# Performance work log

Hardware: AMD Instinct MI355X
Metric: run time of the kernel (lower is better)

## Reference

```python
import jax, jax.numpy as jnp
import numpy as np

NEG = 1e12  # matches the torch '-inf' surrogate value


def _sinusoidal_pos(seq_len, dim):
    # bert4keras-style: pe[..., 0::2] = sin, pe[..., 1::2] = cos
    pos = jnp.arange(seq_len, dtype=jnp.float32)
    i = jnp.arange(dim // 2, dtype=jnp.float32)
    freq = jnp.power(10000.0, -2.0 * i / dim)
    ang = pos[:, None] * freq[None, :]                      # [S, dim/2]
    pe = jnp.stack([jnp.sin(ang), jnp.cos(ang)], axis=-1)   # [S, dim/2, 2]
    return pe.reshape(seq_len, dim)                          # [S, dim]


def _rope(e, cos_pos, sin_pos):
    # additional_part = stack([-e[...,1::2], e[...,::2]], -1).reshape(e.shape)
    rot = jnp.stack([-e[..., 1::2], e[..., 0::2]], axis=-1).reshape(e.shape)
    return e * cos_pos + rot * sin_pos


def setup_inputs() -> dict:
    key = jax.random.key(0)
    k = jax.random.split(key, 5)
    B, S, H, inner, L = 8, 512, 768, 64, 16
    x = jax.random.normal(k[0], (B, S, H), dtype=jnp.float32)
    W1 = jax.random.normal(k[1], (H, 2 * inner), dtype=jnp.float32) * 0.02
    b1 = jnp.zeros((2 * inner,), dtype=jnp.float32)
    W2 = jax.random.normal(k[2], (H, 2 * L), dtype=jnp.float32) * 0.02
    b2 = jnp.zeros((2 * L,), dtype=jnp.float32)
    attention_mask = jnp.ones((B, S), dtype=jnp.int32)
    return {"x": x, "W1": W1, "b1": b1, "W2": W2, "b2": b2,
            "attention_mask": attention_mask}


def reference(x, W1, b1, W2, b2, attention_mask):
    B, S, H = x.shape
    inner = W1.shape[1] // 2

    t = x @ W1 + b1                                 # [B,S,2*inner]
    start_token = t[..., 0::2]                      # [B,S,inner]
    end_token = t[..., 1::2]                        # [B,S,inner]

    pe = _sinusoidal_pos(S, inner)[None]            # [1,S,inner]
    cos_pos = jnp.repeat(pe[..., 1::2], 2, axis=-1)
    sin_pos = jnp.repeat(pe[..., 0::2], 2, axis=-1)
    start_token = _rope(start_token, cos_pos, sin_pos)
    end_token = _rope(end_token, cos_pos, sin_pos)

    span_score = jnp.einsum('bmd,bnd->bmn', start_token, end_token) / (inner ** 0.5)

    typing = jnp.swapaxes(x @ W2 + b2, 1, 2) / 2.0  # [B,2L,S]

    # entity_score: [B, L, S(start), S(end)]
    entity_score = (span_score[:, None]
                    + typing[:, 0::2, None, :]
                    + typing[:, 1::2, :, None])

    m = attention_mask.astype(entity_score.dtype)
    m_row = m[:, None, :, None]                     # mask over start axis
    m_col = m[:, None, None, :]                     # mask over end axis
    entity_score = entity_score * m_row + (-NEG) * (1.0 - m_row)
    entity_score = entity_score * m_col + (-NEG) * (1.0 - m_col)

    tril = jnp.tril(jnp.ones((S, S), entity_score.dtype), k=-1)
    entity_score = entity_score - tril * NEG
    return entity_score
```

## Files before the change

kernel.cpp:

```cpp
#include <hip/hip_runtime.h>

#define NEGF 1.0e12f

constexpr int Hdim = 768;
constexpr int NC   = 160;
constexpr int ROWS = 4096;
constexpr int SEQ  = 512;
constexpr int KSPLIT = 4;

typedef __attribute__((ext_vector_type(8))) short  short8;
typedef __attribute__((ext_vector_type(4))) float  floatx4;

__device__ inline unsigned short f2bf(float f) {
    union { float f; unsigned u; } v; v.f = f;
    return (unsigned short)((v.u + 0x8000u) >> 16);
}

__global__ __launch_bounds__(256) void gemm_mfma_k(
    const float* __restrict__ x, const float* __restrict__ W1,
    const float* __restrict__ W2, float* __restrict__ partial)
{
    __shared__ __align__(16) unsigned short xs[64 * 40];
    __shared__ __align__(16) unsigned short ws[NC * 40];

    const int tid  = threadIdx.x;
    const int wave = tid >> 6;
    const int lane = tid & 63;
    const int quad = lane >> 4;
    const int nl   = lane & 15;
    const int r0   = blockIdx.x * 64;
    const int k0   = blockIdx.y * 192;

    floatx4 acc[10];
#pragma unroll
    for (int t = 0; t < 10; t++) acc[t] = (floatx4)(0.0f);

    for (int kt = 0; kt < 192; kt += 32) {
        const int kb = k0 + kt;
        {
            const int row = tid >> 2;
            const int kq  = (tid & 3) * 8;
            const float* xp = x + (size_t)(r0 + row) * Hdim + kb + kq;
            float4 v0 = *(const float4*)xp;
            float4 v1 = *(const float4*)(xp + 4);
            short8 sv;
            sv[0] = (short)f2bf(v0.x); sv[1] = (short)f2bf(v0.y);
            sv[2] = (short)f2bf(v0.z); sv[3] = (short)f2bf(v0.w);
            sv[4] = (short)f2bf(v1.x); sv[5] = (short)f2bf(v1.y);
            sv[6] = (short)f2bf(v1.z); sv[7] = (short)f2bf(v1.w);
            *(short8*)(xs + row * 40 + kq) = sv;
        }
#pragma unroll
        for (int g = 0; g < 3; g++) {
            const int c   = g * 64 + (tid & 63);
            const int kq2 = (tid >> 6) * 8;
            if (c < NC) {
                float f[8];
                if (c < 128) {
                    const float* wp = W1 + (size_t)(kb + kq2) * 128 + c;
#pragma unroll
                    for (int j = 0; j < 8; j++) f[j] = wp[j * 128];
                } else {
                    const float* wp = W2 + (size_t)(kb + kq2) * 32 + (c - 128);
#pragma unroll
                    for (int j = 0; j < 8; j++) f[j] = wp[j * 32];
                }
                short8 sv;
#pragma unroll
                for (int j = 0; j < 8; j++) sv[j] = (short)f2bf(f[j]);
                *(short8*)(ws + c * 40 + kq2) = sv;
            }
        }
        __syncthreads();

        short8 af = *(const short8*)(xs + (wave * 16 + nl) * 40 + quad * 8);
#pragma unroll
        for (int t = 0; t < 10; t++) {
            short8 bf = *(const short8*)(ws + (t * 16 + nl) * 40 + quad * 8);
            acc[t] = __builtin_amdgcn_mfma_f32_16x16x32_bf16(af, bf, acc[t], 0, 0, 0);
        }
        __syncthreads();
    }

    float* pout = partial + (size_t)blockIdx.y * ROWS * NC;
#pragma unroll
    for (int t = 0; t < 10; t++) {
#pragma unroll
        for (int r = 0; r < 4; r++) {
            pout[(size_t)(r0 + wave * 16 + quad * 4 + r) * NC + t * 16 + nl] = acc[t][r];
        }
    }
}

__global__ __launch_bounds__(256) void combine_rope_k(
    const float* __restrict__ partial, const float* __restrict__ b1,
    const float* __restrict__ b2, unsigned short* __restrict__ startbf,
    unsigned short* __restrict__ endbf, float* __restrict__ tyn,
    float* __restrict__ tym)
{
    const int tid = threadIdx.x;
    const int row = blockIdx.x * 4 + (tid >> 6);
    const int u   = tid & 63;
    const int b   = row >> 9;
    const int s   = row & 511;
    const float* p0 = partial + (size_t)row * NC;
    const size_t cstride = (size_t)ROWS * NC;

    if (u < 32) {
        const int i = u;
        float4 a0 = *(const float4*)(p0 + 4 * i);
        float4 a1 = *(const float4*)(p0 + cstride + 4 * i);
        float4 a2 = *(const float4*)(p0 + 2 * cstride + 4 * i);
        float4 a3 = *(const float4*)(p0 + 3 * cstride + 4 * i);
        float t0 = a0.x + a1.x + a2.x + a3.x + b1[4 * i + 0];
        float t1 = a0.y + a1.y + a2.y + a3.y + b1[4 * i + 1];
        float t2 = a0.z + a1.z + a2.z + a3.z + b1[4 * i + 2];
        float t3 = a0.w + a1.w + a2.w + a3.w + b1[4 * i + 3];
        float freq = __powf(10000.0f, -(float)i * (1.0f / 32.0f));
        float ang  = (float)s * freq;
        float sn, cs;
        __sincosf(ang, &sn, &cs);
        float so0 = (t0 * cs - t2 * sn) * 0.125f;
        float so1 = (t2 * cs + t0 * sn) * 0.125f;
        float eo0 = t1 * cs - t3 * sn;
        float eo1 = t3 * cs + t1 * sn;
        ushort2 sp; sp.x = f2bf(so0); sp.y = f2bf(so1);
        ushort2 ep; ep.x = f2bf(eo0); ep.y = f2bf(eo1);
        *(ushort2*)(startbf + (size_t)row * 64 + 2 * i) = sp;
        *(ushort2*)(endbf   + (size_t)row * 64 + 2 * i) = ep;
    } else {
        const int j = u - 32;
        float t = p0[128 + j] + p0[cstride + 128 + j] + p0[2 * cstride + 128 + j]
                + p0[3 * cstride + 128 + j] + b2[j];
        float v = t * 0.5f;
        const int l = j >> 1;
        if ((j & 1) == 0) tyn[((size_t)b * 16 + l) * SEQ + s] = v;
        else              tym[((size_t)b * 16 + l) * SEQ + s] = v;
    }
}

__global__ __launch_bounds__(256) void entity_k(
    const unsigned short* __restrict__ startbf, const unsigned short* __restrict__ endbf,
    const float* __restrict__ tyn, const float* __restrict__ tym,
    const int* __restrict__ amask, float* __restrict__ out)
{
    __shared__ __align__(16) unsigned short sA[64 * 72];
    __shared__ __align__(16) unsigned short sB[64 * 72];
    __shared__ float tyn_s[16 * 64];
    __shared__ float tym_s[16 * 64];
    __shared__ float mrow_s[64];
    __shared__ float mcol_s[64];

    const int tid = threadIdx.x;
    const int b   = blockIdx.z;
    const int m0  = blockIdx.y * 64;
    const int n0  = blockIdx.x * 64;

    for (int t = tid; t < 512; t += 256) {
        int row = t >> 3;
        int kq  = (t & 7) * 8;
        *(short8*)(sA + row * 72 + kq) =
            *(const short8*)(startbf + (size_t)(b * SEQ + m0 + row) * 64 + kq);
        *(short8*)(sB + row * 72 + kq) =
            *(const short8*)(endbf + (size_t)(b * SEQ + n0 + row) * 64 + kq);
    }
    for (int t = tid; t < 16 * 64; t += 256) {
        int l = t >> 6, i = t & 63;
        tym_s[t] = tym[((size_t)b * 16 + l) * SEQ + m0 + i];
        tyn_s[t] = tyn[((size_t)b * 16 + l) * SEQ + n0 + i];
    }
    if (tid < 64)       mrow_s[tid] = (float)amask[b * SEQ + m0 + tid];
    else if (tid < 128) mcol_s[tid - 64] = (float)amask[b * SEQ + n0 + (tid - 64)];
    __syncthreads();

    const int wave = tid >> 6;
    const int lane = tid & 63;
    const int quad = lane >> 4;
    const int nl   = lane & 15;

    short8 a0 = *(const short8*)(sA + (wave * 16 + nl) * 72 + quad * 8);
    short8 a1 = *(const short8*)(sA + (wave * 16 + nl) * 72 + 32 + quad * 8);

    floatx4 acc[4];
#pragma unroll
    for (int t = 0; t < 4; t++) acc[t] = (floatx4)(0.0f);
#pragma unroll
    for (int t = 0; t < 4; t++) {
        short8 bf0 = *(const short8*)(sB + (t * 16 + nl) * 72 + quad * 8);
        short8 bf1 = *(const short8*)(sB + (t * 16 + nl) * 72 + 32 + quad * 8);
        acc[t] = __builtin_amdgcn_mfma_f32_16x16x32_bf16(a0, bf0, acc[t], 0, 0, 0);
        acc[t] = __builtin_amdgcn_mfma_f32_16x16x32_bf16(a1, bf1, acc[t], 0, 0, 0);
    }

    float mr[4], radd[4];
#pragma unroll
    for (int r = 0; r < 4; r++) {
        mr[r]   = mrow_s[wave * 16 + quad * 4 + r];
        radd[r] = -NEGF * (1.0f - mr[r]);
    }
    float mc[4], cadd[4];
#pragma unroll
    for (int t = 0; t < 4; t++) {
        mc[t]   = mcol_s[t * 16 + nl];
        cadd[t] = -NEGF * (1.0f - mc[t]);
    }
    const bool lower = (m0 > n0);
    const bool diag  = (m0 == n0);
    const int  lm    = wave * 16 + quad * 4;

    for (int l = 0; l < 16; l++) {
        float tmv[4];
#pragma unroll
        for (int r = 0; r < 4; r++) tmv[r] = tym_s[l * 64 + lm + r];
        float* ob = out + ((size_t)(b * 16 + l) * SEQ + m0 + lm) * SEQ + n0;
#pragma unroll
        for (int t = 0; t < 4; t++) {
            float tnv = tyn_s[l * 64 + t * 16 + nl];
#pragma unroll
            for (int r = 0; r < 4; r++) {
                float v = acc[t][r] + tnv + tmv[r];
                v = v * mr[r] + radd[r];
                v = v * mc[t] + cadd[t];
                if (lower) v -= NEGF;
                else if (diag && (lm + r > t * 16 + nl)) v -= NEGF;
                ob[(size_t)r * SEQ + t * 16 + nl] = v;
            }
        }
    }
}

extern "C" void kernel_launch(void* const* d_in, const int* in_sizes, int n_in,
                              void* d_out, int out_size, void* d_ws, size_t ws_size,
                              hipStream_t stream) {
    const float* x     = (const float*)d_in[0];
    const float* W1    = (const float*)d_in[1];
    const float* b1    = (const float*)d_in[2];
    const float* W2    = (const float*)d_in[3];
    const float* b2    = (const float*)d_in[4];
    const int*   amask = (const int*)d_in[5];
    float* out = (float*)d_out;

    char* base = (char*)d_ws;
    float*          partial = (float*)base;
    unsigned short* startbf = (unsigned short*)(base + 10485760);
    unsigned short* endbf   = (unsigned short*)(base + 10485760 + 524288);
    float*          tyn     = (float*)(base + 10485760 + 2 * 524288);
    float*          tym     = (float*)(base + 10485760 + 2 * 524288 + 262144);

    hipLaunchKernelGGL(gemm_mfma_k, dim3(64, KSPLIT), dim3(256), 0, stream,
                       x, W1, W2, partial);
    hipLaunchKernelGGL(combine_rope_k, dim3(ROWS / 4), dim3(256), 0, stream,
                       partial, b1, b2, startbf, endbf, tyn, tym);
    hipLaunchKernelGGL(entity_k, dim3(8, 8, 8), dim3(256), 0, stream,
                       startbf, endbf, tyn, tym, amask, out);
}
```

Baseline: 168.2 us.

## Fuse projection GEMM with RoPE epilogue, drop split-K, and prefetch operands

Replaces the split-K GEMM plus a separate combine/RoPE kernel with one kernel. Each block covers 32 rows over the full K dimension, register-prefetches the next K tile while doing MFMA on the current one, and applies bias, RoPE and typing in an LDS epilogue. This removes the 10MB partial-sum round trip and one launch, but leaves only 128 blocks, which may underfill the GPU. The entity output writes also become nontemporal stores.

```diff
diff --git a/kernel.cpp b/kernel.cpp
--- a/kernel.cpp
+++ b/kernel.cpp
@@ -6,7 +6,6 @@
 constexpr int NC   = 160;
 constexpr int ROWS = 4096;
 constexpr int SEQ  = 512;
-constexpr int KSPLIT = 4;
 
 typedef __attribute__((ext_vector_type(8))) short  short8;
 typedef __attribute__((ext_vector_type(4))) float  floatx4;
@@ -16,126 +15,133 @@
     return (unsigned short)((v.u + 0x8000u) >> 16);
 }
 
-__global__ __launch_bounds__(256) void gemm_mfma_k(
+__global__ __launch_bounds__(256) void gemm_rope_fused_k(
     const float* __restrict__ x, const float* __restrict__ W1,
-    const float* __restrict__ W2, float* __restrict__ partial)
+    const float* __restrict__ b1, const float* __restrict__ W2,
+    const float* __restrict__ b2, unsigned short* __restrict__ startbf,
+    unsigned short* __restrict__ endbf, float* __restrict__ tyn,
+    float* __restrict__ tym)
 {
-    __shared__ __align__(16) unsigned short xs[64 * 40];
+    __shared__ __align__(16) unsigned short xs[32 * 40];
     __shared__ __align__(16) unsigned short ws[NC * 40];
+    __shared__ __align__(16) float ts[32 * 160];
 
     const int tid  = threadIdx.x;
     const int wave = tid >> 6;
     const int lane = tid & 63;
     const int quad = lane >> 4;
     const int nl   = lane & 15;
-    const int r0   = blockIdx.x * 64;
-    const int k0   = blockIdx.y * 192;
-
-    floatx4 acc[10];
-#pragma unroll
-    for (int t = 0; t < 10; t++) acc[t] = (floatx4)(0.0f);
-
-    for (int kt = 0; kt < 192; kt += 32) {
-        const int kb = k0 + kt;
+    const int rg   = wave >> 1;
+    const int cgp  = wave & 1;
+    const int r0   = blockIdx.x * 32;
+
+    const int c0  = tid % 160,         kq0 = (tid / 160) * 8;
+    const int c1  = (tid + 256) % 160, kq1 = ((tid + 256) / 160) * 8;
+    const int c2  = (tid + 512) % 160, kq2 = ((tid + 512) / 160) * 8;
+    const int xrow = tid >> 3;
+    const int xk4  = (tid & 7) * 4;
+
+    floatx4 acc[5];
+#pragma unroll
+    for (int t = 0; t < 5; t++) acc[t] = (floatx4)(0.0f);
+
+    float4 xv;
+    float  wf0[8], wf1[8], wf2[8];
+
+    auto loadW8 = [&](int c, int kq, int kb, float* f) {
+        if (c < 128) {
+            const float* wp = W1 + (size_t)(kb + kq) * 128 + c;
+#pragma unroll
+            for (int j = 0; j < 8; j++) f[j] = wp[(size_t)j * 128];
+        } else {
+            const float* wp = W2 + (size_t)(kb + kq) * 32 + (c - 128);
+#pragma unroll
+            for (int j = 0; j < 8; j++) f[j] = wp[(size_t)j * 32];
+        }
+    };
+
+    xv = *(const float4*)(x + (size_t)(r0 + xrow) * Hdim + 0 + xk4);
+    loadW8(c0, kq0, 0, wf0);
+    loadW8(c1, kq1, 0, wf1);
+    if (tid < 128) loadW8(c2, kq2, 0, wf2);
+
+    for (int kt = 0; kt < 24; kt++) {
         {
-            const int row = tid >> 2;
-            const int kq  = (tid & 3) * 8;
-            const float* xp = x + (size_t)(r0 + row) * Hdim + kb + kq;
-            float4 v0 = *(const float4*)xp;
-            float4 v1 = *(const float4*)(xp + 4);
-            short8 sv;
-            sv[0] = (short)f2bf(v0.x); sv[1] = (short)f2bf(v0.y);
-            sv[2] = (short)f2bf(v0.z); sv[3] = (short)f2bf(v0.w);
-            sv[4] = (short)f2bf(v1.x); sv[5] = (short)f2bf(v1.y);
-            sv[6] = (short)f2bf(v1.z); sv[7] = (short)f2bf(v1.w);
-            *(short8*)(xs + row * 40 + kq) = sv;
-        }
-#pragma unroll
-        for (int g = 0; g < 3; g++) {
-            const int c   = g * 64 + (tid & 63);
-            const int kq2 = (tid >> 6) * 8;
-            if (c < NC) {
-                float f[8];
-                if (c < 128) {
-                    const float* wp = W1 + (size_t)(kb + kq2) * 128 + c;
-#pragma unroll
-                    for (int j = 0; j < 8; j++) f[j] = wp[j * 128];
-                } else {
-                    const float* wp = W2 + (size_t)(kb + kq2) * 32 + (c - 128);
-#pragma unroll
-                    for (int j = 0; j < 8; j++) f[j] = wp[j * 32];
-                }
-                short8 sv;
-#pragma unroll
-                for (int j = 0; j < 8; j++) sv[j] = (short)f2bf(f[j]);
-                *(short8*)(ws + c * 40 + kq2) = sv;
+            short4 sv;
+            sv.x = (short)f2bf(xv.x); sv.y = (short)f2bf(xv.y);
+            sv.z = (short)f2bf(xv.z); sv.w = (short)f2bf(xv.w);
+            *(short4*)(xs + xrow * 40 + xk4) = sv;
+            short8 s0, s1, s2;
+#pragma unroll
+            for (int j = 0; j < 8; j++) { s0[j] = (short)f2bf(wf0[j]); s1[j] = (short)f2bf(wf1[j]); }
+            *(short8*)(ws + c0 * 40 + kq0) = s0;
+            *(short8*)(ws + c1 * 40 + kq1) = s1;
+            if (tid < 128) {
+#pragma unroll
+                for (int j = 0; j < 8; j++) s2[j] = (short)f2bf(wf2[j]);
+                *(short8*)(ws + c2 * 40 + kq2) = s2;
             }
         }
         __syncthreads();
 
-        short8 af = *(const short8*)(xs + (wave * 16 + nl) * 40 + quad * 8);
-#pragma unroll
-        for (int t = 0; t < 10; t++) {
-            short8 bf = *(const short8*)(ws + (t * 16 + nl) * 40 + quad * 8);
+        if (kt < 23) {
+            const int kb = (kt + 1) * 32;
+            xv = *(const float4*)(x + (size_t)(r0 + xrow) * Hdim + kb + xk4);
+            loadW8(c0, kq0, kb, wf0);
+            loadW8(c1, kq1, kb, wf1);
+            if (tid < 128) loadW8(c2, kq2, kb, wf2);
+        }
+
+        short8 af = *(const short8*)(xs + (rg * 16 + nl) * 40 + quad * 8);
+#pragma unroll
+        for (int t = 0; t < 5; t++) {
+            short8 bf = *(const short8*)(ws + ((cgp * 5 + t) * 16 + nl) * 40 + quad * 8);
             acc[t] = __builtin_amdgcn_mfma_f32_16x16x32_bf16(af, bf, acc[t], 0, 0, 0);
         }
         __syncthreads();
     }
 
-    float* pout = partial + (size_t)blockIdx.y * ROWS * NC;
-#pragma unroll
-    for (int t = 0; t < 10; t++) {
+#pragma unroll
+    for (int t = 0; t < 5; t++) {
 #pragma unroll
         for (int r = 0; r < 4; r++) {
-            pout[(size_t)(r0 + wave * 16 + quad * 4 + r) * NC + t * 16 + nl] = acc[t][r];
-        }
-    }
-}
-
-__global__ __launch_bounds__(256) void combine_rope_k(
-    const float* __restrict__ partial, const float* __restrict__ b1,
-    const float* __restrict__ b2, unsigned short* __restrict__ startbf,
-    unsigned short* __restrict__ endbf, float* __restrict__ tyn,
-    float* __restrict__ tym)
-{
-    const int tid = threadIdx.x;
-    const int row = blockIdx.x * 4 + (tid >> 6);
-    const int u   = tid & 63;
-    const int b   = row >> 9;
-    const int s   = row & 511;
-    const float* p0 = partial + (size_t)row * NC;
-    const size_t cstride = (size_t)ROWS * NC;
-
-    if (u < 32) {
-        const int i = u;
-        float4 a0 = *(const float4*)(p0 + 4 * i);
-        float4 a1 = *(const float4*)(p0 + cstride + 4 * i);
-        float4 a2 = *(const float4*)(p0 + 2 * cstride + 4 * i);
-        float4 a3 = *(const float4*)(p0 + 3 * cstride + 4 * i);
-        float t0 = a0.x + a1.x + a2.x + a3.x + b1[4 * i + 0];
-        float t1 = a0.y + a1.y + a2.y + a3.y + b1[4 * i + 1];
-        float t2 = a0.z + a1.z + a2.z + a3.z + b1[4 * i + 2];
-        float t3 = a0.w + a1.w + a2.w + a3.w + b1[4 * i + 3];
-        float freq = __powf(10000.0f, -(float)i * (1.0f / 32.0f));
-        float ang  = (float)s * freq;
-        float sn, cs;
-        __sincosf(ang, &sn, &cs);
-        float so0 = (t0 * cs - t2 * sn) * 0.125f;
-        float so1 = (t2 * cs + t0 * sn) * 0.125f;
-        float eo0 = t1 * cs - t3 * sn;
-        float eo1 = t3 * cs + t1 * sn;
-        ushort2 sp; sp.x = f2bf(so0); sp.y = f2bf(so1);
-        ushort2 ep; ep.x = f2bf(eo0); ep.y = f2bf(eo1);
-        *(ushort2*)(startbf + (size_t)row * 64 + 2 * i) = sp;
-        *(ushort2*)(endbf   + (size_t)row * 64 + 2 * i) = ep;
-    } else {
-        const int j = u - 32;
-        float t = p0[128 + j] + p0[cstride + 128 + j] + p0[2 * cstride + 128 + j]
-                + p0[3 * cstride + 128 + j] + b2[j];
-        float v = t * 0.5f;
-        const int l = j >> 1;
-        if ((j & 1) == 0) tyn[((size_t)b * 16 + l) * SEQ + s] = v;
-        else              tym[((size_t)b * 16 + l) * SEQ + s] = v;
+            ts[(rg * 16 + quad * 4 + r) * 160 + (cgp * 5 + t) * 16 + nl] = acc[t][r];
+        }
+    }
+    __syncthreads();
+
+    for (int idx = tid; idx < 32 * 64; idx += 256) {
+        const int lrow = idx >> 6;
+        const int u    = idx & 63;
+        const int grow = r0 + lrow;
+        const int b    = grow >> 9;
+        const int s    = grow & 511;
+        if (u < 32) {
+            const int i = u;
+            float4 tv = *(const float4*)(ts + lrow * 160 + 4 * i);
+            float4 bv = *(const float4*)(b1 + 4 * i);
+            float t0 = tv.x + bv.x, t1 = tv.y + bv.y;
+            float t2 = tv.z + bv.z, t3 = tv.w + bv.w;
+            float freq = __powf(10000.0f, -(float)i * (1.0f / 32.0f));
+            float ang  = (float)s * freq;
+            float sn, cs;
+            __sincosf(ang, &sn, &cs);
+            float so0 = (t0 * cs - t2 * sn) * 0.125f;
+            float so1 = (t2 * cs + t0 * sn) * 0.125f;
+            float eo0 = t1 * cs - t3 * sn;
+            float eo1 = t3 * cs + t1 * sn;
+            ushort2 sp; sp.x = f2bf(so0); sp.y = f2bf(so1);
+            ushort2 ep; ep.x = f2bf(eo0); ep.y = f2bf(eo1);
+            *(ushort2*)(startbf + (size_t)grow * 64 + 2 * i) = sp;
+            *(ushort2*)(endbf   + (size_t)grow * 64 + 2 * i) = ep;
+        } else {
+            const int j = u - 32;
+            float t = ts[lrow * 160 + 128 + j] + b2[j];
+            float v = t * 0.5f;
+            const int l = j >> 1;
+            if ((j & 1) == 0) tyn[((size_t)b * 16 + l) * SEQ + s] = v;
+            else              tym[((size_t)b * 16 + l) * SEQ + s] = v;
+        }
     }
 }
 
@@ -223,7 +229,7 @@
                 v = v * mc[t] + cadd[t];
                 if (lower) v -= NEGF;
                 else if (diag && (lm + r > t * 16 + nl)) v -= NEGF;
-                ob[(size_t)r * SEQ + t * 16 + nl] = v;
+                __builtin_nontemporal_store(v, ob + (size_t)r * SEQ + t * 16 + nl);
             }
         }
     }
@@ -241,16 +247,13 @@
     float* out = (float*)d_out;
 
     char* base = (char*)d_ws;
-    float*          partial = (float*)base;
-    unsigned short* startbf = (unsigned short*)(base + 10485760);
-    unsigned short* endbf   = (unsigned short*)(base + 10485760 + 524288);
-    float*          tyn     = (float*)(base + 10485760 + 2 * 524288);
-    float*          tym     = (float*)(base + 10485760 + 2 * 524288 + 262144);
-
-    hipLaunchKernelGGL(gemm_mfma_k, dim3(64, KSPLIT), dim3(256), 0, stream,
-                       x, W1, W2, partial);
-    hipLaunchKernelGGL(combine_rope_k, dim3(ROWS / 4), dim3(256), 0, stream,
-                       partial, b1, b2, startbf, endbf, tyn, tym);
+    unsigned short* startbf = (unsigned short*)base;
+    unsigned short* endbf   = (unsigned short*)(base + 524288);
+    float*          tyn     = (float*)(base + 2 * 524288);
+    float*          tym     = (float*)(base + 2 * 524288 + 262144);
+
+    hipLaunchKernelGGL(gemm_rope_fused_k, dim3(128), dim3(256), 0, stream,
+                       x, W1, b1, W2, b2, startbf, endbf, tyn, tym);
     hipLaunchKernelGGL(entity_k, dim3(8, 8, 8), dim3(256), 0, stream,
                        startbf, endbf, tyn, tym, amask, out);
 }
```

New measurement: 219.0 us. +30.2%, slower.
